# Performance work log

Measured on AMD Instinct MI355X. Metric: run time of the kernel, lower is better.

Reference implementation:

```python
import jax, jax.numpy as jnp
import numpy as np

B, S, D, H = 2, 2048, 1024, 16
HD = D // H


def setup_inputs() -> dict:
    key = jax.random.key(0)
    ks = jax.random.split(key, 9)
    sc = 0.02
    return {
        "x": jax.random.normal(ks[0], (B, S, D), dtype=jnp.float32),
        "qw": jax.random.normal(ks[1], (D, D), dtype=jnp.float32) * sc,
        "qb": jax.random.normal(ks[2], (D,), dtype=jnp.float32) * sc,
        "kw": jax.random.normal(ks[3], (D, D), dtype=jnp.float32) * sc,
        "kb": jax.random.normal(ks[4], (D,), dtype=jnp.float32) * sc,
        "vw": jax.random.normal(ks[5], (D, D), dtype=jnp.float32) * sc,
        "vb": jax.random.normal(ks[6], (D,), dtype=jnp.float32) * sc,
        "ow": jax.random.normal(ks[7], (D, D), dtype=jnp.float32) * sc,
        "ob": jax.random.normal(ks[8], (D,), dtype=jnp.float32) * sc,
    }


def reference(x, qw, qb, kw, kb, vw, vb, ow, ob):
    b, s, d = x.shape
    # projections (torch Linear: x @ W.T + b)
    q = (x @ qw.T + qb).reshape(b, s, H, HD).transpose(0, 2, 1, 3)  # bhsd
    k = (x @ kw.T + kb).reshape(b, s, H, HD).transpose(0, 2, 1, 3)
    v = (x @ vw.T + vb).reshape(b, s, H, HD).transpose(0, 2, 1, 3)
    scale = 1.0 / jnp.sqrt(jnp.float32(HD))
    score = jnp.einsum("bhsd,bhtd->bhst", q, k) * scale  # bhss
    # causal mask: -inf strictly above diagonal
    mask = jnp.triu(jnp.full((s, s), -jnp.inf, dtype=score.dtype), k=1)
    score = jax.nn.softmax(score + mask, axis=-1)
    o = jnp.einsum("bhst,bhtd->bhsd", score, v)
    o = o.transpose(0, 2, 1, 3).reshape(b, s, d)
    return o @ ow.T + ob
```

## Files before the change

### kernel.cpp

```cpp
#include <hip/hip_runtime.h>
#include <hip/hip_bf16.h>
#include <stdint.h>

typedef __bf16 bf16x8 __attribute__((ext_vector_type(8)));
typedef __bf16 bf16x4 __attribute__((ext_vector_type(4)));
typedef float f32x4 __attribute__((ext_vector_type(4)));
typedef unsigned short ushort_t;


__device__ inline ushort_t f2bf(float f) {
  union { float f; uint32_t u; } v; v.f = f;
  uint32_t r = (v.u + 0x7fffu + ((v.u >> 16) & 1u)) >> 16;
  return (ushort_t)r;
}

__device__ inline void gll16(const void* g, void* l) {
  __builtin_amdgcn_global_load_lds((const __attribute__((address_space(1))) void*)g,
                                   (__attribute__((address_space(3))) void*)l, 16, 0, 0);
}

__global__ void cvt_x(const float* __restrict__ in, ushort_t* __restrict__ out) {
  int i = blockIdx.x * blockDim.x + threadIdx.x;
  float4 f = ((const float4*)in)[i];
  union { ushort_t u[4]; uint2 v; } r;
  r.u[0] = f2bf(f.x); r.u[1] = f2bf(f.y); r.u[2] = f2bf(f.z); r.u[3] = f2bf(f.w);
  ((uint2*)out)[i] = r.v;
}
__global__ void cvt_w(const float* __restrict__ a, const float* __restrict__ b,
                      const float* __restrict__ c, const float* __restrict__ d,
                      ushort_t* __restrict__ out) {
  const float* srcs[4] = {a, b, c, d};
  const float* s = srcs[blockIdx.y];
  ushort_t* o = out + (size_t)blockIdx.y * 1048576;
  int i = blockIdx.x * blockDim.x + threadIdx.x;
  float4 f = ((const float4*)s)[i];
  union { ushort_t u[4]; uint2 v; } r;
  r.u[0] = f2bf(f.x); r.u[1] = f2bf(f.y); r.u[2] = f2bf(f.z); r.u[3] = f2bf(f.w);
  ((uint2*)(o))[i] = r.v;
}

__global__ __launch_bounds__(256) void qkv_gemm(
    const ushort_t* __restrict__ xb,
    const ushort_t* __restrict__ qwb, const ushort_t* __restrict__ kwb, const ushort_t* __restrict__ vwb,
    const float* __restrict__ qbias, const float* __restrict__ kbias, const float* __restrict__ vbias,
    ushort_t* __restrict__ qo, ushort_t* __restrict__ ko, ushort_t* __restrict__ vto)
{
  const int z = blockIdx.z;
  const float* bias = (z == 0) ? qbias : (z == 1) ? kbias : vbias;
  const ushort_t* Ap;
  const ushort_t* Bp;
  int m0, n0;
  if (z == 2) {
    Ap = vwb; Bp = xb;
    m0 = blockIdx.x * 128;
    n0 = blockIdx.y * 128;
  } else {
    Ap = xb; Bp = (z == 0) ? qwb : kwb;
    m0 = blockIdx.y * 128;
    n0 = blockIdx.x * 128;
  }

  __shared__ __align__(16) ushort_t As[128 * 64];
  __shared__ __align__(16) ushort_t Bs[128 * 64];

  const int tid = threadIdx.x;
  const int w = tid >> 6;
  const int lane = tid & 63;
  const int ln = lane & 15;
  const int q4 = lane >> 4;
  const int wm = w & 1, wn = w >> 1;

  f32x4 acc[4][4];
  #pragma unroll
  for (int i = 0; i < 4; i++)
    #pragma unroll
    for (int j = 0; j < 4; j++) acc[i][j] = f32x4{0.f, 0.f, 0.f, 0.f};

  for (int k0 = 0; k0 < 1024; k0 += 64) {
    __syncthreads();
    #pragma unroll
    for (int i = 0; i < 4; i++) {
      int c = tid + i * 256;
      int row = c >> 3;
      int cq = (c & 7) ^ (row & 7);
      gll16(&Ap[(size_t)(m0 + row) * 1024 + k0 + cq * 8], &As[c * 8]);
      gll16(&Bp[(size_t)(n0 + row) * 1024 + k0 + cq * 8], &Bs[c * 8]);
    }
    __syncthreads();
    #pragma unroll
    for (int ks = 0; ks < 2; ks++) {
      bf16x8 af[4], bfr[4];
      #pragma unroll
      for (int t = 0; t < 4; t++) {
        int rr = wm * 64 + t * 16 + ln;
        af[t]  = *(const bf16x8*)(&As[rr * 64 + (((ks * 4 + q4) ^ (rr & 7)) * 8)]);
        int rc = wn * 64 + t * 16 + ln;
        bfr[t] = *(const bf16x8*)(&Bs[rc * 64 + (((ks * 4 + q4) ^ (rc & 7)) * 8)]);
      }
      #pragma unroll
      for (int tm = 0; tm < 4; tm++)
        #pragma unroll
        for (int tn = 0; tn < 4; tn++)
          acc[tm][tn] = __builtin_amdgcn_mfma_f32_16x16x32_bf16(af[tm], bfr[tn], acc[tm][tn], 0, 0, 0);
    }
  }

  if (z == 2) {
    #pragma unroll
    for (int tn = 0; tn < 4; tn++) {
      int col = n0 + wn * 64 + tn * 16 + ln;
      int bb = col >> 11, s = col & 2047;
      size_t base = (size_t)bb * 2097152 + s;
      #pragma unroll
      for (int tm = 0; tm < 4; tm++) {
        int prow = m0 + wm * 64 + tm * 16 + q4 * 4;
        #pragma unroll
        for (int r = 0; r < 4; r++) {
          int p = prow + r;
          vto[base + (size_t)p * 2048] = f2bf(acc[tm][tn][r] + bias[p]);
        }
      }
    }
  } else {
    #pragma unroll
    for (int tn = 0; tn < 4; tn++) {
      int col = n0 + wn * 64 + tn * 16 + ln;
      float bv = bias[col];
      int h = col >> 6, hd = col & 63;
      #pragma unroll
      for (int tm = 0; tm < 4; tm++) {
        int rowb = m0 + wm * 64 + tm * 16 + q4 * 4;
        #pragma unroll
        for (int r = 0; r < 4; r++) {
          int row = rowb + r;
          int b = row >> 11, s = row & 2047;
          float val = acc[tm][tn][r] + bv;
          if (z == 0) {
            qo[((size_t)((b * 16 + h) * 2048 + s)) * 64 + hd] = f2bf(val * 0.180336884f);
          } else {
            ko[((size_t)((b * 16 + h) * 2048 + s)) * 64 + hd] = f2bf(val);
          }
        }
      }
    }
  }
}

#define PAD 72
#define PPAD 68
__global__ __launch_bounds__(256) void attn(
    const ushort_t* __restrict__ qp, const ushort_t* __restrict__ kp,
    const ushort_t* __restrict__ vtp, ushort_t* __restrict__ op)
{
  __shared__ __align__(16) ushort_t Ks[64 * PAD];
  __shared__ __align__(16) ushort_t Vts[64 * PAD];
  __shared__ __align__(16) ushort_t Ps[8][16 * PPAD];

  const int tid = threadIdx.x;
  const int w = tid >> 6;
  const int lane = tid & 63;
  const int ln = lane & 15;
  const int q4 = lane >> 4;
  const int bh = blockIdx.y;
  const int b = bh >> 4, h = bh & 15;
  int tswz = (blockIdx.x + blockIdx.y) & 15;
  const int qt = (blockIdx.y & 16) ? (15 - tswz) : tswz;
  const int q0 = qt * 128;
  const int nt = 2 * qt + 2;

  const int c0 = tid, c1 = tid + 256;
  const int kr0_row = c0 >> 3, kr0_col = (c0 & 7) * 8;
  const int kr1_row = c1 >> 3, kr1_col = (c1 & 7) * 8;

  bf16x8 onesf;
  {
    union { ushort_t u[8]; bf16x8 v; } t;
    #pragma unroll
    for (int j = 0; j < 8; j++) t.u[j] = 0x3F80;
    onesf = t.v;
  }

  bf16x8 qf[2][2];
  #pragma unroll
  for (int s = 0; s < 2; s++) {
    const ushort_t* base = qp + ((size_t)bh * 2048 + q0 + w * 32 + s * 16 + ln) * 64 + q4 * 8;
    qf[s][0] = *(const bf16x8*)(base);
    qf[s][1] = *(const bf16x8*)(base + 32);
  }

  f32x4 acc_o[2][4];
  f32x4 acc_l[2];
  #pragma unroll
  for (int s = 0; s < 2; s++) {
    acc_l[s] = f32x4{0.f, 0.f, 0.f, 0.f};
    #pragma unroll
    for (int t = 0; t < 4; t++) acc_o[s][t] = f32x4{0.f, 0.f, 0.f, 0.f};
  }

  uint4 kr0, kr1, vr0, vr1;
  {
    const ushort_t* kb = kp + (size_t)bh * 2048 * 64;
    kr0 = *(const uint4*)(kb + kr0_row * 64 + kr0_col);
    kr1 = *(const uint4*)(kb + kr1_row * 64 + kr1_col);
    const ushort_t* vb = vtp + (size_t)bh * 64 * 2048;
    vr0 = *(const uint4*)(vb + (size_t)kr0_row * 2048 + kr0_col);
    vr1 = *(const uint4*)(vb + (size_t)kr1_row * 2048 + kr1_col);
  }

  for (int it = 0; it < nt; it++) {
    if (it) __syncthreads();
    *(uint4*)(&Ks [kr0_row * PAD + kr0_col]) = kr0;
    *(uint4*)(&Ks [kr1_row * PAD + kr1_col]) = kr1;
    *(uint4*)(&Vts[kr0_row * PAD + kr0_col]) = vr0;
    *(uint4*)(&Vts[kr1_row * PAD + kr1_col]) = vr1;
    __syncthreads();

    if (it + 1 < nt) {
      int kv1 = (it + 1) * 64;
      const ushort_t* kb = kp + ((size_t)bh * 2048 + kv1) * 64;
      kr0 = *(const uint4*)(kb + kr0_row * 64 + kr0_col);
      kr1 = *(const uint4*)(kb + kr1_row * 64 + kr1_col);
      const ushort_t* vb = vtp + (size_t)bh * 64 * 2048;
      vr0 = *(const uint4*)(vb + (size_t)kr0_row * 2048 + kv1 + kr0_col);
      vr1 = *(const uint4*)(vb + (size_t)kr1_row * 2048 + kv1 + kr1_col);
    }

    f32x4 sc[2][4];
    #pragma unroll
    for (int s = 0; s < 2; s++)
      #pragma unroll
      for (int t = 0; t < 4; t++) sc[s][t] = f32x4{0.f, 0.f, 0.f, 0.f};
    #pragma unroll
    for (int ks = 0; ks < 2; ks++) {
      bf16x8 kf[4];
      #pragma unroll
      for (int tn = 0; tn < 4; tn++)
        kf[tn] = *(const bf16x8*)(&Ks[(tn * 16 + ln) * PAD + ks * 32 + q4 * 8]);
      #pragma unroll
      for (int s = 0; s < 2; s++)
        #pragma unroll
        for (int tn = 0; tn < 4; tn++)
          sc[s][tn] = __builtin_amdgcn_mfma_f32_16x16x32_bf16(qf[s][ks], kf[tn], sc[s][tn], 0, 0, 0);
    }
    if (it >= 2 * qt) {
      int kv0 = it * 64;
      #pragma unroll
      for (int s = 0; s < 2; s++) {
        int qrow = q0 + w * 32 + s * 16 + q4 * 4;
        #pragma unroll
        for (int tn = 0; tn < 4; tn++) {
          int col = kv0 + tn * 16 + ln;
          #pragma unroll
          for (int r = 0; r < 4; r++)
            if (col > qrow + r) sc[s][tn][r] = -__builtin_inff();
        }
      }
    }
    #pragma unroll
    for (int s = 0; s < 2; s++)
      #pragma unroll
      for (int tn = 0; tn < 4; tn++)
        #pragma unroll
        for (int r = 0; r < 4; r++) {
          float p = __builtin_amdgcn_exp2f(sc[s][tn][r]);
          Ps[w * 2 + s][(q4 * 4 + r) * PPAD + tn * 16 + ln] = (ushort_t)(__float_as_uint(p) >> 16);
        }
    #pragma unroll
    for (int ks = 0; ks < 2; ks++) {
      bf16x8 vf[4];
      #pragma unroll
      for (int tn = 0; tn < 4; tn++)
        vf[tn] = *(const bf16x8*)(&Vts[(tn * 16 + ln) * PAD + ks * 32 + q4 * 8]);
      #pragma unroll
      for (int s = 0; s < 2; s++) {
        const ushort_t* pp = &Ps[w * 2 + s][ln * PPAD + ks * 32 + q4 * 8];
        bf16x4 plo = *(const bf16x4*)(pp);
        bf16x4 phi = *(const bf16x4*)(pp + 4);
        bf16x8 pf = __builtin_shufflevector(plo, phi, 0, 1, 2, 3, 4, 5, 6, 7);
        acc_l[s] = __builtin_amdgcn_mfma_f32_16x16x32_bf16(pf, onesf, acc_l[s], 0, 0, 0);
        #pragma unroll
        for (int tn = 0; tn < 4; tn++)
          acc_o[s][tn] = __builtin_amdgcn_mfma_f32_16x16x32_bf16(pf, vf[tn], acc_o[s][tn], 0, 0, 0);
      }
    }
  }

  #pragma unroll
  for (int s = 0; s < 2; s++) {
    float invl[4];
    #pragma unroll
    for (int r = 0; r < 4; r++) invl[r] = __builtin_amdgcn_rcpf(acc_l[s][r]);
    #pragma unroll
    for (int tn = 0; tn < 4; tn++)
      #pragma unroll
      for (int r = 0; r < 4; r++) {
        int row = q0 + w * 32 + s * 16 + q4 * 4 + r;
        op[((size_t)b * 2048 + row) * 1024 + h * 64 + tn * 16 + ln] =
            f2bf(acc_o[s][tn][r] * invl[r]);
      }
  }
}

__global__ __launch_bounds__(256) void out_gemm(
    const ushort_t* __restrict__ ob_in, const ushort_t* __restrict__ owb,
    const float* __restrict__ obias, float* __restrict__ out)
{
  __shared__ __align__(16) ushort_t As[64 * 64];
  __shared__ __align__(16) ushort_t Bs[128 * 64];

  const int tid = threadIdx.x;
  const int w = tid >> 6;
  const int lane = tid & 63;
  const int ln = lane & 15;
  const int q4 = lane >> 4;
  const int wm = w & 1, wn = w >> 1;
  const int m0 = blockIdx.y * 64;
  const int n0 = blockIdx.x * 128;

  f32x4 acc[2][4];
  #pragma unroll
  for (int i = 0; i < 2; i++)
    #pragma unroll
    for (int j = 0; j < 4; j++) acc[i][j] = f32x4{0.f, 0.f, 0.f, 0.f};

  for (int k0 = 0; k0 < 1024; k0 += 64) {
    __syncthreads();
    #pragma unroll
    for (int i = 0; i < 2; i++) {
      int c = tid + i * 256;
      int row = c >> 3;
      int cq = (c & 7) ^ (row & 7);
      gll16(&ob_in[(size_t)(m0 + row) * 1024 + k0 + cq * 8], &As[c * 8]);
    }
    #pragma unroll
    for (int i = 0; i < 4; i++) {
      int c = tid + i * 256;
      int row = c >> 3;
      int cq = (c & 7) ^ (row & 7);
      gll16(&owb[(size_t)(n0 + row) * 1024 + k0 + cq * 8], &Bs[c * 8]);
    }
    __syncthreads();
    #pragma unroll
    for (int ks = 0; ks < 2; ks++) {
      bf16x8 af[2], bfr[4];
      #pragma unroll
      for (int t = 0; t < 2; t++) {
        int rr = wm * 32 + t * 16 + ln;
        af[t] = *(const bf16x8*)(&As[rr * 64 + (((ks * 4 + q4) ^ (rr & 7)) * 8)]);
      }
      #pragma unroll
      for (int t = 0; t < 4; t++) {
        int rc = wn * 64 + t * 16 + ln;
        bfr[t] = *(const bf16x8*)(&Bs[rc * 64 + (((ks * 4 + q4) ^ (rc & 7)) * 8)]);
      }
      #pragma unroll
      for (int tm = 0; tm < 2; tm++)
        #pragma unroll
        for (int tn = 0; tn < 4; tn++)
          acc[tm][tn] = __builtin_amdgcn_mfma_f32_16x16x32_bf16(af[tm], bfr[tn], acc[tm][tn], 0, 0, 0);
    }
  }

  #pragma unroll
  for (int tn = 0; tn < 4; tn++) {
    int col = n0 + wn * 64 + tn * 16 + ln;
    float bv = obias[col];
    #pragma unroll
    for (int tm = 0; tm < 2; tm++) {
      int rowb = m0 + wm * 32 + tm * 16 + q4 * 4;
      #pragma unroll
      for (int r = 0; r < 4; r++)
        out[(size_t)(rowb + r) * 1024 + col] = acc[tm][tn][r] + bv;
    }
  }
}

extern "C" void kernel_launch(void* const* d_in, const int* in_sizes, int n_in,
                              void* d_out, int out_size, void* d_ws, size_t ws_size,
                              hipStream_t stream) {
  const float* x     = (const float*)d_in[0];
  const float* qw    = (const float*)d_in[1];
  const float* qb    = (const float*)d_in[2];
  const float* kw    = (const float*)d_in[3];
  const float* kb    = (const float*)d_in[4];
  const float* vw    = (const float*)d_in[5];
  const float* vb    = (const float*)d_in[6];
  const float* ow    = (const float*)d_in[7];
  const float* obias = (const float*)d_in[8];
  float* out = (float*)d_out;

  char* ws = (char*)d_ws;
  ushort_t* xb  = (ushort_t*)(ws);
  ushort_t* wb  = (ushort_t*)(ws + 8388608);
  ushort_t* qwb = wb;
  ushort_t* kwb = wb + 1048576;
  ushort_t* vwb = wb + 2097152;
  ushort_t* owb = wb + 3145728;
  ushort_t* qo  = (ushort_t*)(ws + 16777216);
  ushort_t* ko  = (ushort_t*)(ws + 25165824);
  ushort_t* vto = (ushort_t*)(ws + 33554432);
  ushort_t* oo  = (ushort_t*)(ws + 41943040);

  cvt_x<<<dim3(4096), dim3(256), 0, stream>>>(x, xb);
  cvt_w<<<dim3(1024, 4), dim3(256), 0, stream>>>(qw, kw, vw, ow, wb);

  qkv_gemm<<<dim3(8, 32, 3), dim3(256), 0, stream>>>(xb, qwb, kwb, vwb, qb, kb, vb, qo, ko, vto);
  attn<<<dim3(16, 32), dim3(256), 0, stream>>>(qo, ko, vto, oo);
  out_gemm<<<dim3(8, 64), dim3(256), 0, stream>>>(oo, owb, obias, out);
}
```

Before: 192.2 us.

## Fuse x fp32-to-bf16 conversion into QKV GEMM with register-prefetched loads

Removes the separate cvt_x kernel: the QKV GEMM now reads fp32 x directly, converts it to bf16 in registers, and stores it into LDS. Both GEMMs replace direct global-to-LDS loads with register prefetch of the next K tile, which overlaps the global fetch with the MFMA loop. This saves a launch plus a write and re-read of bf16 x. In exchange each of the 24 QKV column tiles re-reads fp32 x, doubling that read traffic, and register pressure rises under the new launch bound of 3.

```diff
diff --git a/kernel.cpp b/kernel.cpp
--- a/kernel.cpp
+++ b/kernel.cpp
@@ -14,18 +14,15 @@
   return (ushort_t)r;
 }
 
-__device__ inline void gll16(const void* g, void* l) {
-  __builtin_amdgcn_global_load_lds((const __attribute__((address_space(1))) void*)g,
-                                   (__attribute__((address_space(3))) void*)l, 16, 0, 0);
-}
-
-__global__ void cvt_x(const float* __restrict__ in, ushort_t* __restrict__ out) {
-  int i = blockIdx.x * blockDim.x + threadIdx.x;
-  float4 f = ((const float4*)in)[i];
-  union { ushort_t u[4]; uint2 v; } r;
-  r.u[0] = f2bf(f.x); r.u[1] = f2bf(f.y); r.u[2] = f2bf(f.z); r.u[3] = f2bf(f.w);
-  ((uint2*)out)[i] = r.v;
-}
+__device__ inline uint4 pack8(const float4& a, const float4& b) {
+  union { __hip_bfloat162 h[4]; uint4 v; } pk;
+  pk.h[0] = __float22bfloat162_rn(float2{a.x, a.y});
+  pk.h[1] = __float22bfloat162_rn(float2{a.z, a.w});
+  pk.h[2] = __float22bfloat162_rn(float2{b.x, b.y});
+  pk.h[3] = __float22bfloat162_rn(float2{b.z, b.w});
+  return pk.v;
+}
+
 __global__ void cvt_w(const float* __restrict__ a, const float* __restrict__ b,
                       const float* __restrict__ c, const float* __restrict__ d,
                       ushort_t* __restrict__ out) {
@@ -39,29 +36,25 @@
   ((uint2*)(o))[i] = r.v;
 }
 
-__global__ __launch_bounds__(256) void qkv_gemm(
-    const ushort_t* __restrict__ xb,
+__global__ __launch_bounds__(256, 3) void qkv_gemm(
+    const float* __restrict__ x,
     const ushort_t* __restrict__ qwb, const ushort_t* __restrict__ kwb, const ushort_t* __restrict__ vwb,
     const float* __restrict__ qbias, const float* __restrict__ kbias, const float* __restrict__ vbias,
     ushort_t* __restrict__ qo, ushort_t* __restrict__ ko, ushort_t* __restrict__ vto)
 {
   const int z = blockIdx.z;
   const float* bias = (z == 0) ? qbias : (z == 1) ? kbias : vbias;
-  const ushort_t* Ap;
-  const ushort_t* Bp;
+  const ushort_t* Wsrc = (z == 0) ? qwb : (z == 1) ? kwb : vwb;
   int m0, n0;
-  if (z == 2) {
-    Ap = vwb; Bp = xb;
-    m0 = blockIdx.x * 128;
-    n0 = blockIdx.y * 128;
-  } else {
-    Ap = xb; Bp = (z == 0) ? qwb : kwb;
-    m0 = blockIdx.y * 128;
-    n0 = blockIdx.x * 128;
-  }
+  if (z == 2) { m0 = blockIdx.x * 128; n0 = blockIdx.y * 128; }
+  else        { m0 = blockIdx.y * 128; n0 = blockIdx.x * 128; }
 
   __shared__ __align__(16) ushort_t As[128 * 64];
   __shared__ __align__(16) ushort_t Bs[128 * 64];
+  ushort_t* XLds = (z == 2) ? Bs : As;
+  ushort_t* WLds = (z == 2) ? As : Bs;
+  const int xrow0 = (z == 2) ? n0 : m0;
+  const int wrow0 = (z == 2) ? m0 : n0;
 
   const int tid = threadIdx.x;
   const int w = tid >> 6;
@@ -70,23 +63,52 @@
   const int q4 = lane >> 4;
   const int wm = w & 1, wn = w >> 1;
 
+  int srow[4], sg[4];
+  #pragma unroll
+  for (int i = 0; i < 4; i++) {
+    int c = tid + i * 256;
+    srow[i] = c >> 3;
+    sg[i] = (c & 7) ^ (srow[i] & 7);
+  }
+
   f32x4 acc[4][4];
   #pragma unroll
   for (int i = 0; i < 4; i++)
     #pragma unroll
     for (int j = 0; j < 4; j++) acc[i][j] = f32x4{0.f, 0.f, 0.f, 0.f};
+
+  float4 fx[8];
+  uint4 wreg[4];
+
+  #pragma unroll
+  for (int i = 0; i < 4; i++) {
+    const float* xs = &x[(size_t)(xrow0 + srow[i]) * 1024 + sg[i] * 8];
+    fx[2 * i] = *(const float4*)xs;
+    fx[2 * i + 1] = *(const float4*)(xs + 4);
+    wreg[i] = *(const uint4*)(&Wsrc[(size_t)(wrow0 + srow[i]) * 1024 + sg[i] * 8]);
+  }
 
   for (int k0 = 0; k0 < 1024; k0 += 64) {
     __syncthreads();
     #pragma unroll
     for (int i = 0; i < 4; i++) {
       int c = tid + i * 256;
-      int row = c >> 3;
-      int cq = (c & 7) ^ (row & 7);
-      gll16(&Ap[(size_t)(m0 + row) * 1024 + k0 + cq * 8], &As[c * 8]);
-      gll16(&Bp[(size_t)(n0 + row) * 1024 + k0 + cq * 8], &Bs[c * 8]);
+      *(uint4*)(&XLds[c * 8]) = pack8(fx[2 * i], fx[2 * i + 1]);
+      *(uint4*)(&WLds[c * 8]) = wreg[i];
     }
     __syncthreads();
+
+    if (k0 + 64 < 1024) {
+      int kn = k0 + 64;
+      #pragma unroll
+      for (int i = 0; i < 4; i++) {
+        const float* xs = &x[(size_t)(xrow0 + srow[i]) * 1024 + kn + sg[i] * 8];
+        fx[2 * i] = *(const float4*)xs;
+        fx[2 * i + 1] = *(const float4*)(xs + 4);
+        wreg[i] = *(const uint4*)(&Wsrc[(size_t)(wrow0 + srow[i]) * 1024 + kn + sg[i] * 8]);
+      }
+    }
+
     #pragma unroll
     for (int ks = 0; ks < 2; ks++) {
       bf16x8 af[4], bfr[4];
@@ -317,29 +339,50 @@
   const int m0 = blockIdx.y * 64;
   const int n0 = blockIdx.x * 128;
 
+  int arow[2], ag[2], brow[4], bg[4];
+  #pragma unroll
+  for (int i = 0; i < 2; i++) {
+    int c = tid + i * 256;
+    arow[i] = c >> 3; ag[i] = (c & 7) ^ (arow[i] & 7);
+  }
+  #pragma unroll
+  for (int i = 0; i < 4; i++) {
+    int c = tid + i * 256;
+    brow[i] = c >> 3; bg[i] = (c & 7) ^ (brow[i] & 7);
+  }
+
   f32x4 acc[2][4];
   #pragma unroll
   for (int i = 0; i < 2; i++)
     #pragma unroll
     for (int j = 0; j < 4; j++) acc[i][j] = f32x4{0.f, 0.f, 0.f, 0.f};
+
+  uint4 areg[2], breg[4];
+  #pragma unroll
+  for (int i = 0; i < 2; i++)
+    areg[i] = *(const uint4*)(&ob_in[(size_t)(m0 + arow[i]) * 1024 + ag[i] * 8]);
+  #pragma unroll
+  for (int i = 0; i < 4; i++)
+    breg[i] = *(const uint4*)(&owb[(size_t)(n0 + brow[i]) * 1024 + bg[i] * 8]);
 
   for (int k0 = 0; k0 < 1024; k0 += 64) {
     __syncthreads();
     #pragma unroll
-    for (int i = 0; i < 2; i++) {
-      int c = tid + i * 256;
-      int row = c >> 3;
-      int cq = (c & 7) ^ (row & 7);
-      gll16(&ob_in[(size_t)(m0 + row) * 1024 + k0 + cq * 8], &As[c * 8]);
-    }
-    #pragma unroll
-    for (int i = 0; i < 4; i++) {
-      int c = tid + i * 256;
-      int row = c >> 3;
-      int cq = (c & 7) ^ (row & 7);
-      gll16(&owb[(size_t)(n0 + row) * 1024 + k0 + cq * 8], &Bs[c * 8]);
-    }
+    for (int i = 0; i < 2; i++) *(uint4*)(&As[(tid + i * 256) * 8]) = areg[i];
+    #pragma unroll
+    for (int i = 0; i < 4; i++) *(uint4*)(&Bs[(tid + i * 256) * 8]) = breg[i];
     __syncthreads();
+
+    if (k0 + 64 < 1024) {
+      int kn = k0 + 64;
+      #pragma unroll
+      for (int i = 0; i < 2; i++)
+        areg[i] = *(const uint4*)(&ob_in[(size_t)(m0 + arow[i]) * 1024 + kn + ag[i] * 8]);
+      #pragma unroll
+      for (int i = 0; i < 4; i++)
+        breg[i] = *(const uint4*)(&owb[(size_t)(n0 + brow[i]) * 1024 + kn + bg[i] * 8]);
+    }
+
     #pragma unroll
     for (int ks = 0; ks < 2; ks++) {
       bf16x8 af[2], bfr[4];
@@ -390,7 +433,6 @@
   float* out = (float*)d_out;
 
   char* ws = (char*)d_ws;
-  ushort_t* xb  = (ushort_t*)(ws);
   ushort_t* wb  = (ushort_t*)(ws + 8388608);
   ushort_t* qwb = wb;
   ushort_t* kwb = wb + 1048576;
@@ -401,10 +443,9 @@
   ushort_t* vto = (ushort_t*)(ws + 33554432);
   ushort_t* oo  = (ushort_t*)(ws + 41943040);
 
-  cvt_x<<<dim3(4096), dim3(256), 0, stream>>>(x, xb);
   cvt_w<<<dim3(1024, 4), dim3(256), 0, stream>>>(qw, kw, vw, ow, wb);
 
-  qkv_gemm<<<dim3(8, 32, 3), dim3(256), 0, stream>>>(xb, qwb, kwb, vwb, qb, kb, vb, qo, ko, vto);
+  qkv_gemm<<<dim3(8, 32, 3), dim3(256), 0, stream>>>(x, qwb, kwb, vwb, qb, kb, vb, qo, ko, vto);
   attn<<<dim3(16, 32), dim3(256), 0, stream>>>(qo, ko, vto, oo);
   out_gemm<<<dim3(8, 64), dim3(256), 0, stream>>>(oo, owb, obias, out);
 }
```

Result: slower. 307.3 us (+59.9%).

## Double-buffer K/V tiles in attention and merge conversion kernels into one launch

Applied to the files above, without the earlier changes.

The attention kernel now keeps two shared-memory buffers for the K and V^T tiles and alternates between them. This removes the barrier at the top of each iteration that guarded against overwriting a tile still being read. Separately, the x and weight fp32-to-bf16 conversions are merged into a single kernel launch to save one launch. The cost is more LDS per block, which may reduce occupancy for the attention kernel.

```diff
diff --git a/kernel.cpp b/kernel.cpp
--- a/kernel.cpp
+++ b/kernel.cpp
@@ -19,24 +19,26 @@
                                    (__attribute__((address_space(3))) void*)l, 16, 0, 0);
 }
 
-__global__ void cvt_x(const float* __restrict__ in, ushort_t* __restrict__ out) {
+__global__ void cvt_all(const float* __restrict__ qw, const float* __restrict__ kw,
+                        const float* __restrict__ vw, const float* __restrict__ ow,
+                        const float* __restrict__ x,
+                        ushort_t* __restrict__ wb, ushort_t* __restrict__ xb) {
+  int y = blockIdx.y;
+  const float* src;
+  ushort_t* dst;
+  if (y < 4) {
+    const float* srcs[4] = {qw, kw, vw, ow};
+    src = srcs[y];
+    dst = wb + (size_t)y * 1048576;
+  } else {
+    src = x + (size_t)(y - 4) * 1048576;
+    dst = xb + (size_t)(y - 4) * 1048576;
+  }
   int i = blockIdx.x * blockDim.x + threadIdx.x;
-  float4 f = ((const float4*)in)[i];
+  float4 f = ((const float4*)src)[i];
   union { ushort_t u[4]; uint2 v; } r;
   r.u[0] = f2bf(f.x); r.u[1] = f2bf(f.y); r.u[2] = f2bf(f.z); r.u[3] = f2bf(f.w);
-  ((uint2*)out)[i] = r.v;
-}
-__global__ void cvt_w(const float* __restrict__ a, const float* __restrict__ b,
-                      const float* __restrict__ c, const float* __restrict__ d,
-                      ushort_t* __restrict__ out) {
-  const float* srcs[4] = {a, b, c, d};
-  const float* s = srcs[blockIdx.y];
-  ushort_t* o = out + (size_t)blockIdx.y * 1048576;
-  int i = blockIdx.x * blockDim.x + threadIdx.x;
-  float4 f = ((const float4*)s)[i];
-  union { ushort_t u[4]; uint2 v; } r;
-  r.u[0] = f2bf(f.x); r.u[1] = f2bf(f.y); r.u[2] = f2bf(f.z); r.u[3] = f2bf(f.w);
-  ((uint2*)(o))[i] = r.v;
+  ((uint2*)dst)[i] = r.v;
 }
 
 __global__ __launch_bounds__(256) void qkv_gemm(
@@ -152,8 +154,8 @@
     const ushort_t* __restrict__ qp, const ushort_t* __restrict__ kp,
     const ushort_t* __restrict__ vtp, ushort_t* __restrict__ op)
 {
-  __shared__ __align__(16) ushort_t Ks[64 * PAD];
-  __shared__ __align__(16) ushort_t Vts[64 * PAD];
+  __shared__ __align__(16) ushort_t Ks[2][64 * PAD];
+  __shared__ __align__(16) ushort_t Vts[2][64 * PAD];
   __shared__ __align__(16) ushort_t Ps[8][16 * PPAD];
 
   const int tid = threadIdx.x;
@@ -208,11 +210,11 @@
   }
 
   for (int it = 0; it < nt; it++) {
-    if (it) __syncthreads();
-    *(uint4*)(&Ks [kr0_row * PAD + kr0_col]) = kr0;
-    *(uint4*)(&Ks [kr1_row * PAD + kr1_col]) = kr1;
-    *(uint4*)(&Vts[kr0_row * PAD + kr0_col]) = vr0;
-    *(uint4*)(&Vts[kr1_row * PAD + kr1_col]) = vr1;
+    const int buf = it & 1;
+    *(uint4*)(&Ks [buf][kr0_row * PAD + kr0_col]) = kr0;
+    *(uint4*)(&Ks [buf][kr1_row * PAD + kr1_col]) = kr1;
+    *(uint4*)(&Vts[buf][kr0_row * PAD + kr0_col]) = vr0;
+    *(uint4*)(&Vts[buf][kr1_row * PAD + kr1_col]) = vr1;
     __syncthreads();
 
     if (it + 1 < nt) {
@@ -235,7 +237,7 @@
       bf16x8 kf[4];
       #pragma unroll
       for (int tn = 0; tn < 4; tn++)
-        kf[tn] = *(const bf16x8*)(&Ks[(tn * 16 + ln) * PAD + ks * 32 + q4 * 8]);
+        kf[tn] = *(const bf16x8*)(&Ks[buf][(tn * 16 + ln) * PAD + ks * 32 + q4 * 8]);
       #pragma unroll
       for (int s = 0; s < 2; s++)
         #pragma unroll
@@ -270,7 +272,7 @@
       bf16x8 vf[4];
       #pragma unroll
       for (int tn = 0; tn < 4; tn++)
-        vf[tn] = *(const bf16x8*)(&Vts[(tn * 16 + ln) * PAD + ks * 32 + q4 * 8]);
+        vf[tn] = *(const bf16x8*)(&Vts[buf][(tn * 16 + ln) * PAD + ks * 32 + q4 * 8]);
       #pragma unroll
       for (int s = 0; s < 2; s++) {
         const ushort_t* pp = &Ps[w * 2 + s][ln * PPAD + ks * 32 + q4 * 8];
@@ -401,8 +403,7 @@
   ushort_t* vto = (ushort_t*)(ws + 33554432);
   ushort_t* oo  = (ushort_t*)(ws + 41943040);
 
-  cvt_x<<<dim3(4096), dim3(256), 0, stream>>>(x, xb);
-  cvt_w<<<dim3(1024, 4), dim3(256), 0, stream>>>(qw, kw, vw, ow, wb);
+  cvt_all<<<dim3(1024, 8), dim3(256), 0, stream>>>(qw, kw, vw, ow, x, wb, xb);
 
   qkv_gemm<<<dim3(8, 32, 3), dim3(256), 0, stream>>>(xb, qwb, kwb, vwb, qb, kb, vb, qo, ko, vto);
   attn<<<dim3(16, 32), dim3(256), 0, stream>>>(qo, ko, vto, oo);
```

Result: slower. 200.1 us (+4.1%).
